# Kernel tuning notes

Hardware: AMD Instinct MI355X
Metric: run time of the kernel (lower is better)

Reference implementation:

```python
import jax, jax.numpy as jnp
import numpy as np

_SAMPLING_EPS = 1e-5


def setup_inputs() -> dict:
    key = jax.random.key(0)
    k1, k2, k3, k4, k5 = jax.random.split(key, 5)
    B, V = 128, 128000
    logits = jax.random.normal(k1, (B, V), dtype=jnp.float32)
    temperature = jax.random.uniform(k2, (B,), dtype=jnp.float32)  # some rows < eps -> greedy
    top_k = jax.random.randint(k3, (B,), 1, 64, dtype=jnp.int32)   # in [1, 63]
    top_p = jax.random.uniform(k4, (B,), dtype=jnp.float32, minval=0.05, maxval=1.0)
    noise_u = jax.random.uniform(k5, (B, V), dtype=jnp.float32, minval=1e-10, maxval=1.0)
    return {"logits": logits, "temperature": temperature, "top_k": top_k,
            "top_p": top_p, "noise_u": noise_u, "max_num_logprobs": 5}


def _apply_top_k_top_p(logits, k, p):
    # Faithful to vLLM: ascending sort, top-k threshold mask, top-p cumsum mask, scatter back.
    B, V = logits.shape
    order = jnp.argsort(logits, axis=-1)                       # ascending, [B, V]
    logits_sort = jnp.take_along_axis(logits, order, axis=-1)
    neg_inf = jnp.float32(-jnp.inf)
    # top-k: pivot value at position V - k; everything strictly below it -> -inf
    pivot_idx = (V - k.astype(jnp.int32))[:, None]             # [B, 1]
    pivot = jnp.take_along_axis(logits_sort, pivot_idx, axis=-1)
    logits_sort = jnp.where(logits_sort < pivot, neg_inf, logits_sort)
    # top-p: softmax over sorted logits, cumsum, drop prefix with mass <= 1 - p (keep last)
    probs_sort = jax.nn.softmax(logits_sort, axis=-1)
    probs_sum = jnp.cumsum(probs_sort, axis=-1)
    top_p_mask = probs_sum <= (1.0 - p)[:, None]
    top_p_mask = top_p_mask.at[:, -1].set(False)
    logits_sort = jnp.where(top_p_mask, neg_inf, logits_sort)
    # scatter back to original vocab order
    rows = jnp.arange(B)[:, None]
    return jnp.zeros_like(logits).at[rows, order].set(logits_sort)


def reference(logits, temperature, top_k, top_p, noise_u, max_num_logprobs):
    # temperature scaling (temp < eps means greedy; divide by 1.0 instead)
    temp = jnp.where(temperature < _SAMPLING_EPS, 1.0, temperature)
    logits = logits.astype(jnp.float32) / temp[:, None]
    # top-k / top-p filtering
    logits = _apply_top_k_top_p(logits, top_k, top_p)
    # probabilities and sampling
    probs = jax.nn.softmax(logits, axis=-1)
    greedy = jnp.argmax(probs, axis=-1)
    q = -jnp.log(noise_u)                                      # Exp(1) noise (q.exponential_())
    random = jnp.argmax(probs / q, axis=-1)
    sampled = jnp.where(temperature < _SAMPLING_EPS, greedy, random).astype(jnp.int32)
    # top-k logprobs
    logprobs = jax.nn.log_softmax(logits, axis=-1)
    topk_logprobs, topk_indices = jax.lax.top_k(logprobs, max_num_logprobs)
    return sampled, topk_indices.astype(jnp.int32), topk_logprobs
```

## Files before the change

### kernel.cpp

```cpp
#include <hip/hip_runtime.h>
#include <math.h>
#include <stdint.h>

#define BT     256
#define NCHUNK 8
#define CAP    2048
#define TOPC   64
#define TILE   (BT * 8)
#define NC     (NCHUNK * TOPC)

__device__ __forceinline__ unsigned f2ord(float f) {
    unsigned u = __float_as_uint(f);
    return u ^ ((u & 0x80000000u) ? 0xFFFFFFFFu : 0x80000000u);
}
__device__ __forceinline__ float ord2f(unsigned k) {
    unsigned u = (k & 0x80000000u) ? (k ^ 0x80000000u) : (k ^ 0xFFFFFFFFu);
    return __uint_as_float(u);
}

__device__ unsigned radix_select_compact(uint2* s_buf, uint2* s_keep,
                                         unsigned (*s_hist)[16], unsigned* p_cnt2,
                                         unsigned n, int tid, int wid)
{
    unsigned prefix = 0u;
    int remaining = TOPC;
    for (int shift = 28; shift >= 0; shift -= 4) {
        if (tid < 64) ((unsigned*)s_hist)[tid] = 0u;
        __syncthreads();
        for (unsigned i = (unsigned)tid; i < n; i += BT) {
            unsigned k = s_buf[i].x;
            bool ing = (shift == 28) || ((k >> (shift + 4)) == (prefix >> (shift + 4)));
            if (ing) atomicAdd(&s_hist[wid][(k >> shift) & 15u], 1u);
        }
        __syncthreads();
        int cum = 0; int b = 0; unsigned hb = 0u;
        for (int bb = 15; bb >= 0; --bb) {
            unsigned h = s_hist[0][bb] + s_hist[1][bb] + s_hist[2][bb] + s_hist[3][bb];
            cum += (int)h;
            if (cum >= remaining) { b = bb; hb = h; break; }
        }
        remaining -= (cum - (int)hb);
        prefix |= ((unsigned)b) << shift;
        __syncthreads();
    }
    if (tid == 0) *p_cnt2 = 0u;
    __syncthreads();
    for (unsigned i = (unsigned)tid; i < n; i += BT) {
        uint2 c = s_buf[i];
        if (c.x > prefix) {
            unsigned pos = atomicAdd(p_cnt2, 1u);
            s_keep[pos] = c;
        }
    }
    __syncthreads();
    for (unsigned i = (unsigned)tid; i < n; i += BT) {
        uint2 c = s_buf[i];
        if (c.x == prefix) {
            unsigned pos = atomicAdd(p_cnt2, 1u);
            if (pos < TOPC) s_keep[pos] = c;
        }
    }
    __syncthreads();
    return prefix;
}

__global__ __launch_bounds__(BT) void phase1_topk_chunks(
    const float* __restrict__ logits, uint2* __restrict__ cand,
    int V, int chunk_len)
{
    __shared__ uint2    s_buf[CAP];
    __shared__ uint2    s_keep[TOPC];
    __shared__ unsigned s_hist[4][16];
    __shared__ unsigned s_cnt, s_cnt2, s_thr, s_ovf;

    const int row   = blockIdx.y;
    const int chunk = blockIdx.x;
    const int tid   = threadIdx.x;
    const int wid   = tid >> 6;
    const int c0    = chunk * chunk_len;
    int c1 = c0 + chunk_len; if (c1 > V) c1 = V;
    const float* rowp = logits + (size_t)row * (size_t)V;

    if (tid == 0) s_ovf = 0u;

    {
        int base = c0 + tid * 8;
        unsigned k[8];
        if (base < c1) {
            float4 a = *(const float4*)(rowp + base);
            float4 b = *(const float4*)(rowp + base + 4);
            k[0] = f2ord(a.x); k[1] = f2ord(a.y); k[2] = f2ord(a.z); k[3] = f2ord(a.w);
            k[4] = f2ord(b.x); k[5] = f2ord(b.y); k[6] = f2ord(b.z); k[7] = f2ord(b.w);
        } else {
            #pragma unroll
            for (int j = 0; j < 8; ++j) k[j] = 0u;
        }
        #pragma unroll
        for (int j = 0; j < 8; ++j) {
            int id = (base < c1) ? (base + j) : c0;
            s_buf[tid + j * BT] = make_uint2(k[j], (unsigned)id);
        }
    }
    __syncthreads();
    {
        unsigned vst = radix_select_compact(s_buf, s_keep, s_hist, &s_cnt2,
                                            CAP, tid, wid);
        if (tid < TOPC) s_buf[tid] = s_keep[tid];
        if (tid == 0) { s_cnt = TOPC; s_thr = vst; }
        __syncthreads();
    }

    float4 a0 = {}, b0 = {}; bool v0 = false;
    int t0 = c0 + TILE;
    if (t0 < c1) {
        int bs = t0 + tid * 8;
        if (bs < c1) {
            a0 = *(const float4*)(rowp + bs);
            b0 = *(const float4*)(rowp + bs + 4);
            v0 = true;
        }
    }
    for (int t = t0; t < c1; t += TILE) {
        float4 a1 = {}, b1 = {}; bool v1 = false;
        int tn = t + TILE;
        if (tn < c1) {
            int bs = tn + tid * 8;
            if (bs < c1) {
                a1 = *(const float4*)(rowp + bs);
                b1 = *(const float4*)(rowp + bs + 4);
                v1 = true;
            }
        }
        unsigned k[8];
        if (v0) {
            k[0] = f2ord(a0.x); k[1] = f2ord(a0.y); k[2] = f2ord(a0.z); k[3] = f2ord(a0.w);
            k[4] = f2ord(b0.x); k[5] = f2ord(b0.y); k[6] = f2ord(b0.z); k[7] = f2ord(b0.w);
        } else {
            #pragma unroll
            for (int j = 0; j < 8; ++j) k[j] = 0u;
        }
        const int base = t + tid * 8;
        const unsigned thr = s_thr;
        unsigned pm = 0u; int np = 0;
        #pragma unroll
        for (int j = 0; j < 8; ++j)
            if (k[j] > thr) { pm |= (1u << j); ++np; }

        for (;;) {
            if (np) {
                unsigned pos = atomicAdd(&s_cnt, (unsigned)np);
                unsigned rem = 0u; int nr = 0;
                #pragma unroll
                for (int j = 0; j < 8; ++j) {
                    if (pm & (1u << j)) {
                        if (pos < CAP) s_buf[pos] = make_uint2(k[j], (unsigned)(base + j));
                        else { rem |= (1u << j); ++nr; }
                        ++pos;
                    }
                }
                if (nr) s_ovf = 1u;
                pm = rem; np = nr;
            }
            __syncthreads();
            unsigned ovf = s_ovf;
            __syncthreads();
            if (!ovf) break;
            unsigned n = s_cnt; if (n > CAP) n = CAP;
            unsigned v2 = radix_select_compact(s_buf, s_keep, s_hist, &s_cnt2,
                                               n, tid, wid);
            if (tid < TOPC) s_buf[tid] = s_keep[tid];
            if (tid == 0) { s_cnt = TOPC; s_thr = v2; s_ovf = 0u; }
            __syncthreads();
            unsigned rem = 0u; int nr = 0;
            #pragma unroll
            for (int j = 0; j < 8; ++j)
                if ((pm & (1u << j)) && k[j] > v2) { rem |= (1u << j); ++nr; }
            pm = rem; np = nr;
        }
        a0 = a1; b0 = b1; v0 = v1;
    }

    unsigned n = s_cnt;
    radix_select_compact(s_buf, s_keep, s_hist, &s_cnt2, n, tid, wid);
    if (tid < TOPC)
        cand[((size_t)row * NCHUNK + chunk) * TOPC + tid] = s_keep[tid];
}

__global__ __launch_bounds__(BT) void phase2_sample(
    const uint2* __restrict__ cand,
    const float* __restrict__ temperature,
    const int*   __restrict__ top_k,
    const float* __restrict__ top_p,
    const float* __restrict__ noise_u,
    float* __restrict__ out,
    int B, int V, int M)
{
    __shared__ unsigned key[NC];
    __shared__ int      idx[NC];
    __shared__ float    sval[TOPC], se[TOPC], sq[TOPC];
    __shared__ int      sidx[TOPC];

    const int r   = blockIdx.x;
    const int tid = threadIdx.x;

    for (int i = tid; i < NC; i += BT) {
        uint2 c = cand[(size_t)r * NC + i];
        key[i] = c.x; idx[i] = (int)c.y;
    }
    __syncthreads();

    for (int kk = 2; kk <= NC; kk <<= 1) {
        for (int j = kk >> 1; j > 0; j >>= 1) {
            int t  = tid;
            int i0 = ((t & ~(j - 1)) << 1) | (t & (j - 1));
            int i1 = i0 | j;
            bool up = ((i0 & kk) == 0);
            unsigned ka = key[i0], kb = key[i1];
            int ia = idx[i0], ib = idx[i1];
            bool gt = (ka > kb) || (ka == kb && ia < ib);
            if (gt == up) { key[i0] = kb; key[i1] = ka; idx[i0] = ib; idx[i1] = ia; }
            __syncthreads();
        }
    }

    float temp_orig = temperature[r];
    float temp = (temp_orig < 1e-5f) ? 1.0f : temp_orig;

    if (tid < TOPC) {
        unsigned k = key[NC - 1 - tid];
        int id = idx[NC - 1 - tid];
        sval[tid] = ord2f(k) / temp;
        sidx[tid] = id;
        float u = noise_u[(size_t)r * (size_t)V + id];
        sq[tid] = -logf(u);
    }
    __syncthreads();
    if (tid < TOPC) se[tid] = expf(sval[tid] - sval[0]);
    __syncthreads();

    if (tid == 0) {
        int k = top_k[r];
        if (k < 1) k = 1; if (k > TOPC) k = TOPC;
        float p = top_p[r];

        float pivot = sval[k - 1];
        int m = k;
        while (m < TOPC && sval[m] >= pivot) ++m;

        float sum = 0.f;
        for (int i = 0; i < m; ++i) sum += se[i];

        float thr1 = 1.0f - p;
        float S = 0.f;
        int f = 1;
        for (int i = m - 1; i >= 1; --i) {
            S += se[i] / sum;
            if (S > thr1) { f = i + 1; break; }
        }

        float sum2 = 0.f;
        for (int i = 0; i < f; ++i) sum2 += se[i];

        int greedy = sidx[0];
        float best = -1.f; int bidx = 0x7fffffff;
        for (int i = 0; i < f; ++i) {
            float ratio = (se[i] / sum2) / sq[i];
            if (ratio > best || (ratio == best && sidx[i] < bidx)) {
                best = ratio; bidx = sidx[i];
            }
        }
        int sampled = (temp_orig < 1e-5f) ? greedy : bidx;

        float lse = logf(sum2);
        out[r] = (float)sampled;
        float* oidx = out + B + (size_t)r * M;
        float* olp  = out + B + (size_t)B * M + (size_t)r * M;
        int produced = 0;
        for (int i = 0; i < f && produced < M; ++i, ++produced) {
            oidx[produced] = (float)sidx[i];
            olp[produced]  = (sval[i] - sval[0]) - lse;
        }
        int v = 0;
        while (produced < M) {
            bool used = false;
            for (int i = 0; i < f; ++i) if (sidx[i] == v) { used = true; break; }
            if (!used) { oidx[produced] = (float)v; olp[produced] = -3.0e38f; ++produced; }
            ++v;
        }
    }
}

extern "C" void kernel_launch(void* const* d_in, const int* in_sizes, int n_in,
                              void* d_out, int out_size, void* d_ws, size_t ws_size,
                              hipStream_t stream)
{
    const float* logits      = (const float*)d_in[0];
    const float* temperature = (const float*)d_in[1];
    const int*   top_k       = (const int*)d_in[2];
    const float* top_p       = (const float*)d_in[3];
    const float* noise_u     = (const float*)d_in[4];

    const int B = in_sizes[1];
    const int V = in_sizes[0] / B;
    const int M = (out_size / B - 1) / 2;

    uint2* cand = (uint2*)d_ws;

    int chunk_len = (((V + NCHUNK - 1) / NCHUNK) + 7) & ~7;

    dim3 g1(NCHUNK, B);
    phase1_topk_chunks<<<g1, BT, 0, stream>>>(logits, cand, V, chunk_len);
    phase2_sample<<<B, BT, 0, stream>>>(cand, temperature, top_k, top_p, noise_u,
                                        (float*)d_out, B, V, M);
}
```

Measured before the change: 181.9 us.

## Fuse chunk top-k and sampling via last-block counter; 16 chunks, 8-bit radix

Merges the two kernels into one. The last block per row is detected with an atomic counter and does the final merge and sampling. The vocab is split into 16 chunks per row instead of 8 when the workspace allows, for more parallelism. The initial threshold comes from a two-pass 8-bit histogram on the first tile instead of a full radix-select. Radix select switches from 4-bit to 8-bit digits, which means fewer passes. The second launch and the 512-element bitonic sort go away, at the cost of serialized tail work in one block and reliance on per-row counters persisting across calls (modulo arithmetic).

```diff
diff --git a/kernel.cpp b/kernel.cpp
--- a/kernel.cpp
+++ b/kernel.cpp
@@ -3,11 +3,12 @@
 #include <stdint.h>
 
 #define BT     256
-#define NCHUNK 8
+#define TOPC   64
 #define CAP    2048
-#define TOPC   64
 #define TILE   (BT * 8)
-#define NC     (NCHUNK * TOPC)
+#define NCH_HI 16
+#define NCH_LO 8
+#define NC_LO  (NCH_LO * TOPC)
 
 __device__ __forceinline__ unsigned f2ord(float f) {
     unsigned u = __float_as_uint(f);
@@ -18,24 +19,24 @@
     return __uint_as_float(u);
 }
 
-__device__ unsigned radix_select_compact(uint2* s_buf, uint2* s_keep,
-                                         unsigned (*s_hist)[16], unsigned* p_cnt2,
-                                         unsigned n, int tid, int wid)
+__device__ unsigned radix_select_compact8(uint2* s_buf, uint2* s_keep,
+                                          unsigned* s_hist, unsigned* p_cnt2,
+                                          unsigned n, int tid)
 {
     unsigned prefix = 0u;
     int remaining = TOPC;
-    for (int shift = 28; shift >= 0; shift -= 4) {
-        if (tid < 64) ((unsigned*)s_hist)[tid] = 0u;
+    for (int shift = 24; shift >= 0; shift -= 8) {
+        s_hist[tid] = 0u;
         __syncthreads();
         for (unsigned i = (unsigned)tid; i < n; i += BT) {
             unsigned k = s_buf[i].x;
-            bool ing = (shift == 28) || ((k >> (shift + 4)) == (prefix >> (shift + 4)));
-            if (ing) atomicAdd(&s_hist[wid][(k >> shift) & 15u], 1u);
+            bool ing = (shift == 24) || ((k >> (shift + 8)) == (prefix >> (shift + 8)));
+            if (ing) atomicAdd(&s_hist[(k >> shift) & 255u], 1u);
         }
         __syncthreads();
         int cum = 0; int b = 0; unsigned hb = 0u;
-        for (int bb = 15; bb >= 0; --bb) {
-            unsigned h = s_hist[0][bb] + s_hist[1][bb] + s_hist[2][bb] + s_hist[3][bb];
+        for (int bb = 255; bb >= 0; --bb) {
+            unsigned h = s_hist[bb];
             cum += (int)h;
             if (cum >= remaining) { b = bb; hb = h; break; }
         }
@@ -47,10 +48,7 @@
     __syncthreads();
     for (unsigned i = (unsigned)tid; i < n; i += BT) {
         uint2 c = s_buf[i];
-        if (c.x > prefix) {
-            unsigned pos = atomicAdd(p_cnt2, 1u);
-            s_keep[pos] = c;
-        }
+        if (c.x > prefix) s_keep[atomicAdd(p_cnt2, 1u)] = c;
     }
     __syncthreads();
     for (unsigned i = (unsigned)tid; i < n; i += BT) {
@@ -64,88 +62,138 @@
     return prefix;
 }
 
-__global__ __launch_bounds__(BT) void phase1_topk_chunks(
+__global__ __launch_bounds__(BT) void sampler_fused(
     const float* __restrict__ logits, uint2* __restrict__ cand,
-    int V, int chunk_len)
+    unsigned* __restrict__ counters,
+    const float* __restrict__ temperature,
+    const int*   __restrict__ top_k,
+    const float* __restrict__ top_p,
+    const float* __restrict__ noise_u,
+    float* __restrict__ out,
+    int B, int V, int M, int chunk_len, int nchunk)
 {
     __shared__ uint2    s_buf[CAP];
     __shared__ uint2    s_keep[TOPC];
-    __shared__ unsigned s_hist[4][16];
-    __shared__ unsigned s_cnt, s_cnt2, s_thr, s_ovf;
+    __shared__ unsigned s_hist[BT];
+    __shared__ float    sval[TOPC], se[TOPC], sq[TOPC];
+    __shared__ int      sidx[TOPC];
+    __shared__ unsigned s_cnt, s_cnt2, s_thr, s_ovf, s_last;
 
     const int row   = blockIdx.y;
     const int chunk = blockIdx.x;
     const int tid   = threadIdx.x;
-    const int wid   = tid >> 6;
     const int c0    = chunk * chunk_len;
     int c1 = c0 + chunk_len; if (c1 > V) c1 = V;
     const float* rowp = logits + (size_t)row * (size_t)V;
 
-    if (tid == 0) s_ovf = 0u;
-
-    {
-        int base = c0 + tid * 8;
-        unsigned k[8];
-        if (base < c1) {
-            float4 a = *(const float4*)(rowp + base);
-            float4 b = *(const float4*)(rowp + base + 4);
-            k[0] = f2ord(a.x); k[1] = f2ord(a.y); k[2] = f2ord(a.z); k[3] = f2ord(a.w);
-            k[4] = f2ord(b.x); k[5] = f2ord(b.y); k[6] = f2ord(b.z); k[7] = f2ord(b.w);
-        } else {
-            #pragma unroll
-            for (int j = 0; j < 8; ++j) k[j] = 0u;
-        }
+    if (tid == 0) { s_ovf = 0u; s_cnt = 0u; }
+    s_hist[tid] = 0u;
+    __syncthreads();
+
+    unsigned k0[8];
+    const int  base0 = c0 + tid * 8;
+    const bool vld0  = (base0 < c1);
+    if (vld0) {
+        float4 a = *(const float4*)(rowp + base0);
+        float4 b = *(const float4*)(rowp + base0 + 4);
+        k0[0] = f2ord(a.x); k0[1] = f2ord(a.y); k0[2] = f2ord(a.z); k0[3] = f2ord(a.w);
+        k0[4] = f2ord(b.x); k0[5] = f2ord(b.y); k0[6] = f2ord(b.z); k0[7] = f2ord(b.w);
+    } else {
         #pragma unroll
-        for (int j = 0; j < 8; ++j) {
-            int id = (base < c1) ? (base + j) : c0;
-            s_buf[tid + j * BT] = make_uint2(k[j], (unsigned)id);
-        }
-    }
-    __syncthreads();
-    {
-        unsigned vst = radix_select_compact(s_buf, s_keep, s_hist, &s_cnt2,
-                                            CAP, tid, wid);
-        if (tid < TOPC) s_buf[tid] = s_keep[tid];
-        if (tid == 0) { s_cnt = TOPC; s_thr = vst; }
-        __syncthreads();
-    }
-
-    float4 a0 = {}, b0 = {}; bool v0 = false;
-    int t0 = c0 + TILE;
+        for (int j = 0; j < 8; ++j) k0[j] = 0u;
+    }
+
+    float4 pa0 = {}, pb0 = {}; bool v0 = false;
+    const int t0 = c0 + TILE;
     if (t0 < c1) {
         int bs = t0 + tid * 8;
         if (bs < c1) {
-            a0 = *(const float4*)(rowp + bs);
-            b0 = *(const float4*)(rowp + bs + 4);
+            pa0 = *(const float4*)(rowp + bs);
+            pb0 = *(const float4*)(rowp + bs + 4);
             v0 = true;
         }
     }
+
+    if (vld0) {
+        #pragma unroll
+        for (int j = 0; j < 8; ++j) atomicAdd(&s_hist[k0[j] >> 24], 1u);
+    }
+    __syncthreads();
+
+    unsigned thr = 0u;
+    {
+        unsigned cum = 0u, h1 = 0u; int b1 = -1;
+        for (int b = 255; b >= 0; --b) {
+            unsigned h = s_hist[b];
+            cum += h;
+            if (cum >= TOPC) { b1 = b; h1 = h; break; }
+        }
+        const bool have = (b1 >= 0);
+        const unsigned rem2 = have ? (TOPC - (cum - h1)) : 1u;
+        __syncthreads();
+        s_hist[tid] = 0u;
+        __syncthreads();
+        if (vld0 && have) {
+            #pragma unroll
+            for (int j = 0; j < 8; ++j)
+                if ((int)(k0[j] >> 24) == b1)
+                    atomicAdd(&s_hist[(k0[j] >> 16) & 255u], 1u);
+        }
+        __syncthreads();
+        if (have) {
+            unsigned cum2 = 0u; int b2 = 0;
+            for (int b = 255; b >= 0; --b) {
+                cum2 += s_hist[b];
+                if (cum2 >= rem2) { b2 = b; break; }
+            }
+            thr = ((unsigned)b1 << 24) | ((unsigned)b2 << 16);
+        }
+    }
+
+    {
+        unsigned pm = 0u; int np = 0;
+        if (vld0) {
+            #pragma unroll
+            for (int j = 0; j < 8; ++j)
+                if (k0[j] >= thr) { pm |= (1u << j); ++np; }
+        }
+        if (np) {
+            unsigned pos = atomicAdd(&s_cnt, (unsigned)np);
+            #pragma unroll
+            for (int j = 0; j < 8; ++j)
+                if (pm & (1u << j)) s_buf[pos++] = make_uint2(k0[j], (unsigned)(base0 + j));
+        }
+        if (tid == 0) s_thr = thr;
+        __syncthreads();
+    }
+
     for (int t = t0; t < c1; t += TILE) {
-        float4 a1 = {}, b1 = {}; bool v1 = false;
+        float4 pa1 = {}, pb1 = {}; bool v1 = false;
         int tn = t + TILE;
         if (tn < c1) {
             int bs = tn + tid * 8;
             if (bs < c1) {
-                a1 = *(const float4*)(rowp + bs);
-                b1 = *(const float4*)(rowp + bs + 4);
+                pa1 = *(const float4*)(rowp + bs);
+                pb1 = *(const float4*)(rowp + bs + 4);
                 v1 = true;
             }
         }
         unsigned k[8];
         if (v0) {
-            k[0] = f2ord(a0.x); k[1] = f2ord(a0.y); k[2] = f2ord(a0.z); k[3] = f2ord(a0.w);
-            k[4] = f2ord(b0.x); k[5] = f2ord(b0.y); k[6] = f2ord(b0.z); k[7] = f2ord(b0.w);
+            k[0] = f2ord(pa0.x); k[1] = f2ord(pa0.y); k[2] = f2ord(pa0.z); k[3] = f2ord(pa0.w);
+            k[4] = f2ord(pb0.x); k[5] = f2ord(pb0.y); k[6] = f2ord(pb0.z); k[7] = f2ord(pb0.w);
         } else {
             #pragma unroll
             for (int j = 0; j < 8; ++j) k[j] = 0u;
         }
         const int base = t + tid * 8;
-        const unsigned thr = s_thr;
+        const unsigned thr2 = s_thr;
         unsigned pm = 0u; int np = 0;
-        #pragma unroll
-        for (int j = 0; j < 8; ++j)
-            if (k[j] > thr) { pm |= (1u << j); ++np; }
-
+        if (v0) {
+            #pragma unroll
+            for (int j = 0; j < 8; ++j)
+                if (k[j] >= thr2) { pm |= (1u << j); ++np; }
+        }
         for (;;) {
             if (np) {
                 unsigned pos = atomicAdd(&s_cnt, (unsigned)np);
@@ -166,8 +214,7 @@
             __syncthreads();
             if (!ovf) break;
             unsigned n = s_cnt; if (n > CAP) n = CAP;
-            unsigned v2 = radix_select_compact(s_buf, s_keep, s_hist, &s_cnt2,
-                                               n, tid, wid);
+            unsigned v2 = radix_select_compact8(s_buf, s_keep, s_hist, &s_cnt2, n, tid);
             if (tid < TOPC) s_buf[tid] = s_keep[tid];
             if (tid == 0) { s_cnt = TOPC; s_thr = v2; s_ovf = 0u; }
             __syncthreads();
@@ -177,13 +224,118 @@
                 if ((pm & (1u << j)) && k[j] > v2) { rem |= (1u << j); ++nr; }
             pm = rem; np = nr;
         }
-        a0 = a1; b0 = b1; v0 = v1;
-    }
-
-    unsigned n = s_cnt;
-    radix_select_compact(s_buf, s_keep, s_hist, &s_cnt2, n, tid, wid);
+        pa0 = pa1; pb0 = pb1; v0 = v1;
+    }
+
+    {
+        unsigned n = s_cnt; if (n > CAP) n = CAP;
+        if (n < TOPC) {
+            for (unsigned i = n + (unsigned)tid; i < TOPC; i += BT)
+                s_buf[i] = make_uint2(0u, (unsigned)((c0 < V) ? c0 : 0));
+            n = TOPC;
+            __syncthreads();
+        }
+        radix_select_compact8(s_buf, s_keep, s_hist, &s_cnt2, n, tid);
+    }
     if (tid < TOPC)
-        cand[((size_t)row * NCHUNK + chunk) * TOPC + tid] = s_keep[tid];
+        cand[((size_t)row * (unsigned)nchunk + (unsigned)chunk) * TOPC + tid] = s_keep[tid];
+
+    if (counters == nullptr) return;
+
+    __threadfence();
+    __syncthreads();
+    if (tid == 0)
+        s_last = ((atomicAdd(&counters[row], 1u) % (unsigned)nchunk)
+                  == (unsigned)(nchunk - 1)) ? 1u : 0u;
+    __syncthreads();
+    if (!s_last) return;
+    __threadfence();
+
+    const int nc = nchunk * TOPC;
+    for (int i = tid; i < nc; i += BT)
+        s_buf[i] = cand[(size_t)row * nc + i];
+    __syncthreads();
+    radix_select_compact8(s_buf, s_keep, s_hist, &s_cnt2, (unsigned)nc, tid);
+
+    for (int kk = 2; kk <= TOPC; kk <<= 1) {
+        for (int j = kk >> 1; j > 0; j >>= 1) {
+            if (tid < TOPC / 2) {
+                int i0 = ((tid & ~(j - 1)) << 1) | (tid & (j - 1));
+                int i1 = i0 | j;
+                bool up = ((i0 & kk) == 0);
+                uint2 A = s_keep[i0], Bv = s_keep[i1];
+                bool gt = (A.x < Bv.x) || (A.x == Bv.x && A.y > Bv.y);
+                if (gt == up) { s_keep[i0] = Bv; s_keep[i1] = A; }
+            }
+            __syncthreads();
+        }
+    }
+
+    float temp_orig = temperature[row];
+    float temp = (temp_orig < 1e-5f) ? 1.0f : temp_orig;
+
+    if (tid < TOPC) {
+        unsigned k = s_keep[tid].x;
+        int id = (int)s_keep[tid].y;
+        sval[tid] = ord2f(k) / temp;
+        sidx[tid] = id;
+        float u = noise_u[(size_t)row * (size_t)V + id];
+        sq[tid] = -logf(u);
+    }
+    __syncthreads();
+    if (tid < TOPC) se[tid] = expf(sval[tid] - sval[0]);
+    __syncthreads();
+
+    if (tid == 0) {
+        int k = top_k[row];
+        if (k < 1) k = 1; if (k > TOPC) k = TOPC;
+        float p = top_p[row];
+
+        float pivot = sval[k - 1];
+        int m = k;
+        while (m < TOPC && sval[m] >= pivot) ++m;
+
+        float sum = 0.f;
+        for (int i = 0; i < m; ++i) sum += se[i];
+
+        float thr1 = 1.0f - p;
+        float S = 0.f;
+        int f = 1;
+        for (int i = m - 1; i >= 1; --i) {
+            S += se[i] / sum;
+            if (S > thr1) { f = i + 1; break; }
+        }
+
+        float sum2 = 0.f;
+        for (int i = 0; i < f; ++i) sum2 += se[i];
+
+        int greedy = sidx[0];
+        float best = -1.f; int bidx = 0x7fffffff;
+        for (int i = 0; i < f; ++i) {
+            float ratio = (se[i] / sum2) / sq[i];
+            if (ratio > best || (ratio == best && sidx[i] < bidx)) {
+                best = ratio; bidx = sidx[i];
+            }
+        }
+        int sampled = (temp_orig < 1e-5f) ? greedy : bidx;
+
+        float lse = logf(sum2);
+        out[row] = (float)sampled;
+        float* oidx = out + B + (size_t)row * M;
+        float* olp  = out + B + (size_t)B * M + (size_t)row * M;
+        int produced = 0;
+        for (int i = 0; i < f && produced < M; ++i, ++produced) {
+            oidx[produced] = (float)sidx[i];
+            olp[produced]  = (sval[i] - sval[0]) - lse;
+        }
+        int v = 0;
+        while (produced < M) {
+            bool used = false;
+            for (int i = 0; i < f; ++i) if (sidx[i] == v) { used = true; break; }
+            if (!used) { oidx[produced] = (float)v; olp[produced] = -3.0e38f; ++produced; }
+            ++v;
+        }
+    }
 }
 
 __global__ __launch_bounds__(BT) void phase2_sample(
@@ -195,21 +347,21 @@
     float* __restrict__ out,
     int B, int V, int M)
 {
-    __shared__ unsigned key[NC];
-    __shared__ int      idx[NC];
+    __shared__ unsigned key[NC_LO];
+    __shared__ int      idx[NC_LO];
     __shared__ float    sval[TOPC], se[TOPC], sq[TOPC];
     __shared__ int      sidx[TOPC];
 
     const int r   = blockIdx.x;
     const int tid = threadIdx.x;
 
-    for (int i = tid; i < NC; i += BT) {
-        uint2 c = cand[(size_t)r * NC + i];
+    for (int i = tid; i < NC_LO; i += BT) {
+        uint2 c = cand[(size_t)r * NC_LO + i];
         key[i] = c.x; idx[i] = (int)c.y;
     }
     __syncthreads();
 
-    for (int kk = 2; kk <= NC; kk <<= 1) {
+    for (int kk = 2; kk <= NC_LO; kk <<= 1) {
         for (int j = kk >> 1; j > 0; j >>= 1) {
             int t  = tid;
             int i0 = ((t & ~(j - 1)) << 1) | (t & (j - 1));
@@ -227,8 +379,8 @@
     float temp = (temp_orig < 1e-5f) ? 1.0f : temp_orig;
 
     if (tid < TOPC) {
-        unsigned k = key[NC - 1 - tid];
-        int id = idx[NC - 1 - tid];
+        unsigned k = key[NC_LO - 1 - tid];
+        int id = idx[NC_LO - 1 - tid];
         sval[tid] = ord2f(k) / temp;
         sidx[tid] = id;
         float u = noise_u[(size_t)r * (size_t)V + id];
@@ -242,14 +394,11 @@
         int k = top_k[r];
         if (k < 1) k = 1; if (k > TOPC) k = TOPC;
         float p = top_p[r];
-
         float pivot = sval[k - 1];
         int m = k;
         while (m < TOPC && sval[m] >= pivot) ++m;
-
         float sum = 0.f;
         for (int i = 0; i < m; ++i) sum += se[i];
-
         float thr1 = 1.0f - p;
         float S = 0.f;
         int f = 1;
@@ -257,10 +406,8 @@
             S += se[i] / sum;
             if (S > thr1) { f = i + 1; break; }
         }
-
         float sum2 = 0.f;
         for (int i = 0; i < f; ++i) sum2 += se[i];
-
         int greedy = sidx[0];
         float best = -1.f; int bidx = 0x7fffffff;
         for (int i = 0; i < f; ++i) {
@@ -270,7 +417,6 @@
             }
         }
         int sampled = (temp_orig < 1e-5f) ? greedy : bidx;
-
         float lse = logf(sum2);
         out[r] = (float)sampled;
         float* oidx = out + B + (size_t)r * M;
@@ -304,12 +450,27 @@
     const int V = in_sizes[0] / B;
     const int M = (out_size / B - 1) / 2;
 
+    const size_t cand16 = (size_t)B * NCH_HI * TOPC * sizeof(uint2);
+    const size_t cand8  = (size_t)B * NCH_LO * TOPC * sizeof(uint2);
+
+    int nch;
+    bool fused;
+    if (ws_size >= cand16 + (size_t)B * sizeof(unsigned))      { nch = NCH_HI; fused = true; }
+    else if (ws_size >= cand8 + (size_t)B * sizeof(unsigned))  { nch = NCH_LO; fused = true; }
+    else                                                       { nch = NCH_LO; fused = false; }
+
     uint2* cand = (uint2*)d_ws;
-
-    int chunk_len = (((V + NCHUNK - 1) / NCHUNK) + 7) & ~7;
-
-    dim3 g1(NCHUNK, B);
-    phase1_topk_chunks<<<g1, BT, 0, stream>>>(logits, cand, V, chunk_len);
-    phase2_sample<<<B, BT, 0, stream>>>(cand, temperature, top_k, top_p, noise_u,
-                                        (float*)d_out, B, V, M);
-}
+    unsigned* counters = fused
+        ? (unsigned*)((char*)d_ws + (size_t)B * nch * TOPC * sizeof(uint2))
+        : nullptr;
+
+    int chunk_len = (((V + nch - 1) / nch) + 7) & ~7;
+
+    dim3 g1(nch, B);
+    sampler_fused<<<g1, BT, 0, stream>>>(logits, cand, counters, temperature,
+                                         top_k, top_p, noise_u, (float*)d_out,
+                                         B, V, M, chunk_len, nch);
+    if (!fused)
+        phase2_sample<<<B, BT, 0, stream>>>(cand, temperature, top_k, top_p,
+                                            noise_u, (float*)d_out, B, V, M);
+}
```

Result: slower. 332.6 us (+82.8%).
